# Performance work log

Hardware: AMD Instinct MI355X
Metric: run time of the kernel (lower is better)

The kernel has to match this reference:

```python
import jax, jax.numpy as jnp
import numpy as np

N = 50000      # nodes
E = 800000     # edges (avg degree 16)
DIN = 128
DOUT = 128
L = 8          # num GCN2Conv layers
ALPHA = 0.1
THETA = 0.5


def setup_inputs() -> dict:
    key = jax.random.key(0)
    ks = jax.random.split(key, 5)
    x = jax.random.normal(ks[0], (N, DIN), jnp.float32)
    edge_index = jax.random.randint(ks[1], (2, E), 0, N, dtype=jnp.int64)
    # pre-normalized adjacency weights (normalize=False in GCN2Conv -> adj_t already normalized)
    edge_weight = jax.random.uniform(ks[2], (E,), jnp.float32) / 16.0
    W_lin = jax.random.normal(ks[3], (DIN, DOUT), jnp.float32) / np.sqrt(DIN).astype(np.float32)
    b_lin = jnp.zeros((DOUT,), jnp.float32)
    W_convs = jax.random.normal(ks[4], (L, DOUT, DOUT), jnp.float32) / np.sqrt(DOUT).astype(np.float32)
    return {"x": x, "edge_weight": edge_weight, "W_lin": W_lin, "b_lin": b_lin,
            "W_convs": W_convs, "edge_index": edge_index}


def reference(x, edge_weight, W_lin, b_lin, W_convs, edge_index):
    src, dst = edge_index[0], edge_index[1]
    # betas for GCN2Conv layer l (1-indexed): beta_l = log(theta/l + 1)
    betas = np.log(THETA / np.arange(1, L + 1) + 1.0).astype(np.float32)
    # x = lins(x).relu(); dropout p=0 is a no-op
    x0 = jax.nn.relu(x @ W_lin + b_lin)          # [N, DOUT]
    h = x0
    for l in range(L):
        # sparse propagate: agg = A @ h  (SpMM via gather + segment_sum)
        agg = jax.ops.segment_sum(h[src] * edge_weight[:, None], dst, num_segments=N)
        # initial-residual mixing
        m = (1.0 - ALPHA) * agg + ALPHA * x0
        # identity mapping (shared_weights): out = (1-beta)*m + beta*(m @ W)
        h = jax.nn.relu((1.0 - betas[l]) * m + betas[l] * (m @ W_convs[l]))
    return h
```

## Files before the change

kernel.cpp:

```cpp
#include <hip/hip_runtime.h>
#include <math.h>

#define N_NODES 50000
#define N_EDGES 800000
#define DIM 128
#define PAD 120

typedef __attribute__((ext_vector_type(8))) short short8;
typedef __attribute__((ext_vector_type(4))) float floatx4;

__device__ __forceinline__ unsigned short f32_to_bf16(float f) {
    unsigned int u = __float_as_uint(f);
    u += 0x7fffu + ((u >> 16) & 1u);
    return (unsigned short)(u >> 16);
}
__device__ __forceinline__ float bf16_to_f32(unsigned short h) {
    return __uint_as_float((unsigned int)h << 16);
}

__global__ __launch_bounds__(256) void prep(const float* __restrict__ Wlin,
                                            const float* __restrict__ Wcv,
                                            int* __restrict__ cnt,
                                            unsigned short* __restrict__ WTg) {
    int i = blockIdx.x * 256 + threadIdx.x;
    if (i < N_NODES) cnt[i] = 0;
    int m = i >> 14;
    int n = (i >> 7) & 127;
    int k = i & 127;
    float v;
    if (m == 0) {
        v = Wlin[k * 128 + n];
    } else {
        int l = m - 1;
        float beta = logf(0.5f / (float)(l + 1) + 1.0f);
        v = beta * Wcv[(size_t)l * 16384 + k * 128 + n]
            + ((n == k) ? (1.0f - beta) : 0.0f);
    }
    WTg[i] = f32_to_bf16(v);
}

__global__ __launch_bounds__(256) void scatter_pad(const int* __restrict__ src,
                                                   const int* __restrict__ dst,
                                                   const float* __restrict__ ew,
                                                   int* __restrict__ cnt,
                                                   int2* __restrict__ bucket) {
    int e = blockIdx.x * 256 + threadIdx.x;
    if (e < N_EDGES) {
        int d = dst[e];
        int pos = atomicAdd(&cnt[d], 1);
        if (pos < PAD) {
            int2 p; p.x = src[e]; p.y = __float_as_int(ew[e]);
            bucket[(size_t)d * PAD + pos] = p;
        }
    }
}

__global__ __launch_bounds__(256) void gemm_x0(const float* __restrict__ x,
                                               const unsigned short* __restrict__ WTg,
                                               const float* __restrict__ bias,
                                               unsigned short* __restrict__ x0B) {
    __shared__ unsigned short WT[128][136];
    for (int idx = threadIdx.x; idx < 2048; idx += 256) {
        int n = idx >> 4, c = idx & 15;
        *(short8*)(void*)&WT[n][c * 8] =
            *(const short8*)(const void*)(WTg + n * 128 + c * 8);
    }
    __syncthreads();
    int wave = threadIdx.x >> 6;
    int lane = threadIdx.x & 63;
    int r0 = (blockIdx.x * 4 + wave) * 16;
    if (r0 >= N_NODES) return;
    int mrow = lane & 15;
    int quad = lane >> 4;
    floatx4 acc[8];
#pragma unroll
    for (int t = 0; t < 8; t++) acc[t] = {0.f, 0.f, 0.f, 0.f};
#pragma unroll
    for (int k0 = 0; k0 < 128; k0 += 32) {
        const float* arow = x + (size_t)(r0 + mrow) * DIM;
        floatx4 alo = *(const floatx4*)(const void*)(arow + k0 + quad * 8);
        floatx4 ahi = *(const floatx4*)(const void*)(arow + k0 + quad * 8 + 4);
        short8 a;
#pragma unroll
        for (int j = 0; j < 4; j++) a[j] = (short)f32_to_bf16(alo[j]);
#pragma unroll
        for (int j = 0; j < 4; j++) a[4 + j] = (short)f32_to_bf16(ahi[j]);
#pragma unroll
        for (int t = 0; t < 8; t++) {
            short8 b = *(const short8*)(const void*)(&WT[t * 16 + mrow][k0 + quad * 8]);
            acc[t] = __builtin_amdgcn_mfma_f32_16x16x32_bf16(a, b, acc[t], 0, 0, 0);
        }
    }
#pragma unroll
    for (int t = 0; t < 8; t++) {
        int col = t * 16 + mrow;
        float bv = bias[col];
#pragma unroll
        for (int i = 0; i < 4; i++) {
            int row = r0 + quad * 4 + i;
            float v = fmaxf(acc[t][i] + bv, 0.f);
            x0B[(size_t)row * DIM + col] = f32_to_bf16(v);
        }
    }
}

__global__ __launch_bounds__(512, 4) void layer_fused(
        const unsigned short* __restrict__ hB,
        const unsigned short* __restrict__ x0B,
        const int* __restrict__ cnt,
        const int2* __restrict__ bucket,
        const unsigned short* __restrict__ WTg,
        float* __restrict__ outF,
        unsigned short* __restrict__ outB) {
    __shared__ unsigned short WT[128][136];
    __shared__ unsigned short M[32][136];
    int tid = threadIdx.x;
    for (int idx = tid; idx < 2048; idx += 512) {
        int n = idx >> 4, c = idx & 15;
        *(short8*)(void*)&WT[n][c * 8] =
            *(const short8*)(const void*)(WTg + n * 128 + c * 8);
    }
    int wave = tid >> 6;
    int lane = tid & 63;
    int eg = lane >> 4;
    int fb = (lane & 15) * 8;
    int r0 = blockIdx.x * 32;

    for (int s = 0; s < 4; s++) {
        int row = (wave << 2) + s;
        int node = r0 + row;
        float acc[8] = {0.f, 0.f, 0.f, 0.f, 0.f, 0.f, 0.f, 0.f};
        if (node < N_NODES) {
            int end = min(cnt[node], PAD);
            if (end > 0) {
                const int2* ep = bucket + (size_t)node * PAD;
                int last = end - 1;
                for (int i = 0; i < end; i += 16) {
                    int i0 = i + eg, i1 = i0 + 4, i2 = i0 + 8, i3 = i0 + 12;
                    int2 e0 = ep[min(i0, last)];
                    int2 e1 = ep[min(i1, last)];
                    int2 e2 = ep[min(i2, last)];
                    int2 e3 = ep[min(i3, last)];
                    short8 r0v = *(const short8*)(const void*)(hB + (size_t)e0.x * DIM + fb);
                    short8 r1v = *(const short8*)(const void*)(hB + (size_t)e1.x * DIM + fb);
                    short8 r2v = *(const short8*)(const void*)(hB + (size_t)e2.x * DIM + fb);
                    short8 r3v = *(const short8*)(const void*)(hB + (size_t)e3.x * DIM + fb);
                    float w0 = (i0 < end) ? __int_as_float(e0.y) : 0.f;
                    float w1 = (i1 < end) ? __int_as_float(e1.y) : 0.f;
                    float w2 = (i2 < end) ? __int_as_float(e2.y) : 0.f;
                    float w3 = (i3 < end) ? __int_as_float(e3.y) : 0.f;
#pragma unroll
                    for (int j = 0; j < 8; j++) {
                        acc[j] = fmaf(w0, bf16_to_f32((unsigned short)r0v[j]), acc[j]);
                        acc[j] = fmaf(w1, bf16_to_f32((unsigned short)r1v[j]), acc[j]);
                        acc[j] = fmaf(w2, bf16_to_f32((unsigned short)r2v[j]), acc[j]);
                        acc[j] = fmaf(w3, bf16_to_f32((unsigned short)r3v[j]), acc[j]);
                    }
                }
            }
        }
#pragma unroll
        for (int j = 0; j < 8; j++) {
            acc[j] += __shfl_down(acc[j], 32);
            acc[j] += __shfl_down(acc[j], 16);
        }
        if (lane < 16) {
            short8 o;
            if (node < N_NODES) {
                short8 xv = *(const short8*)(const void*)(x0B + (size_t)node * DIM + fb);
#pragma unroll
                for (int j = 0; j < 8; j++)
                    o[j] = (short)f32_to_bf16(0.9f * acc[j]
                                              + 0.1f * bf16_to_f32((unsigned short)xv[j]));
            } else {
#pragma unroll
                for (int j = 0; j < 8; j++) o[j] = 0;
            }
            *(short8*)(void*)&M[row][fb] = o;
        }
    }
    __syncthreads();

    int mrow = lane & 15;
    int quad = lane >> 4;
    int rt = wave >> 2;
    int ctb = (wave & 3) * 2;
    floatx4 acc2[2];
    acc2[0] = {0.f, 0.f, 0.f, 0.f};
    acc2[1] = {0.f, 0.f, 0.f, 0.f};
#pragma unroll
    for (int k0 = 0; k0 < 128; k0 += 32) {
        short8 a = *(const short8*)(const void*)(&M[rt * 16 + mrow][k0 + quad * 8]);
#pragma unroll
        for (int t = 0; t < 2; t++) {
            short8 b = *(const short8*)(const void*)(&WT[(ctb + t) * 16 + mrow][k0 + quad * 8]);
            acc2[t] = __builtin_amdgcn_mfma_f32_16x16x32_bf16(a, b, acc2[t], 0, 0, 0);
        }
    }
#pragma unroll
    for (int t = 0; t < 2; t++) {
        int col = (ctb + t) * 16 + mrow;
#pragma unroll
        for (int i = 0; i < 4; i++) {
            int row = r0 + rt * 16 + quad * 4 + i;
            if (row < N_NODES) {
                float v = fmaxf(acc2[t][i], 0.f);
                size_t off = (size_t)row * DIM + col;
                if (outF) outF[off] = v;
                if (outB) outB[off] = f32_to_bf16(v);
            }
        }
    }
}


extern "C" void kernel_launch(void* const* d_in, const int* in_sizes, int n_in,
                              void* d_out, int out_size, void* d_ws, size_t ws_size,
                              hipStream_t stream) {
    const float* x    = (const float*)d_in[0];
    const float* ew   = (const float*)d_in[1];
    const float* Wlin = (const float*)d_in[2];
    const float* blin = (const float*)d_in[3];
    const float* Wcv  = (const float*)d_in[4];
    const int* eidx = (const int*)d_in[5];
    const int* esrc = eidx;
    const int* edst = eidx + N_EDGES;
    float* out = (float*)d_out;

    char* ws = (char*)d_ws;
    unsigned short* x0B = (unsigned short*)(ws);
    unsigned short* hA  = (unsigned short*)(ws + 12800000);
    unsigned short* hB2 = (unsigned short*)(ws + 25600000);
    int* cnt            = (int*)(ws + 38400000);
    int2* bucket        = (int2*)(ws + 38600064);
    unsigned short* WTg = (unsigned short*)(ws + 86600064);

    prep<<<576, 256, 0, stream>>>(Wlin, Wcv, cnt, WTg);

    scatter_pad<<<(N_EDGES + 255) / 256, 256, 0, stream>>>(esrc, edst, ew, cnt, bucket);

    gemm_x0<<<(N_NODES + 63) / 64, 256, 0, stream>>>(x, WTg, blin, x0B);

    const unsigned short* hin = x0B;
    for (int l = 0; l < 8; l++) {
        unsigned short* hout = (l == 7) ? nullptr : ((l & 1) ? hB2 : hA);
        layer_fused<<<1563, 512, 0, stream>>>(hin, x0B, cnt, bucket,
                                              WTg + (size_t)(1 + l) * 16384,
                                              (l == 7) ? out : nullptr, hout);
        hin = hout;
    }
}
```

Before: 470.6 us.

## Build padded CSR buckets via two-pass binning by destination node block

Replaces the single per-edge atomic scatter into per-node padded buckets with a two-stage approach. Edges are first binned into groups of 64 destination nodes using global atomics. A second kernel then scatters each bin into the per-node buckets using shared-memory atomics. The intent is to cut global atomic contention and scattered writes during graph preprocessing, at the cost of an extra kernel launch and an intermediate buffer aliased onto hA. It also packs the local destination into the high bits of src, which assumes src < 65536 (true for N=50000), and it silently drops edges if a bin exceeds 1536 entries.

```diff
diff --git a/kernel.cpp b/kernel.cpp
--- a/kernel.cpp
+++ b/kernel.cpp
@@ -6,6 +6,11 @@
 #define DIM 128
 #define PAD 120
 
+#define BIN_SHIFT 6
+#define BIN_NODES 64
+#define N_BINS 782
+#define BIN_CAP 1536
+
 typedef __attribute__((ext_vector_type(8))) short short8;
 typedef __attribute__((ext_vector_type(4))) float floatx4;
 
@@ -20,10 +25,10 @@
 
 __global__ __launch_bounds__(256) void prep(const float* __restrict__ Wlin,
                                             const float* __restrict__ Wcv,
-                                            int* __restrict__ cnt,
+                                            int* __restrict__ bc,
                                             unsigned short* __restrict__ WTg) {
     int i = blockIdx.x * 256 + threadIdx.x;
-    if (i < N_NODES) cnt[i] = 0;
+    if (i < N_BINS) bc[i] = 0;
     int m = i >> 14;
     int n = (i >> 7) & 127;
     int k = i & 127;
@@ -39,20 +44,48 @@
     WTg[i] = f32_to_bf16(v);
 }
 
-__global__ __launch_bounds__(256) void scatter_pad(const int* __restrict__ src,
-                                                   const int* __restrict__ dst,
-                                                   const float* __restrict__ ew,
-                                                   int* __restrict__ cnt,
-                                                   int2* __restrict__ bucket) {
+__global__ __launch_bounds__(256) void bin_edges(const int* __restrict__ src,
+                                                 const int* __restrict__ dst,
+                                                 const float* __restrict__ ew,
+                                                 int* __restrict__ bc,
+                                                 int2* __restrict__ binbuf) {
     int e = blockIdx.x * 256 + threadIdx.x;
     if (e < N_EDGES) {
         int d = dst[e];
-        int pos = atomicAdd(&cnt[d], 1);
+        int bin = d >> BIN_SHIFT;
+        int pos = atomicAdd(&bc[bin], 1);
+        if (pos < BIN_CAP) {
+            int2 p;
+            p.x = src[e] | ((d & (BIN_NODES - 1)) << 16);
+            p.y = __float_as_int(ew[e]);
+            binbuf[(size_t)bin * BIN_CAP + pos] = p;
+        }
+    }
+}
+
+__global__ __launch_bounds__(256) void bin_scatter(const int* __restrict__ bc,
+                                                   const int2* __restrict__ binbuf,
+                                                   int* __restrict__ cnt,
+                                                   int2* __restrict__ bucket) {
+    __shared__ int c[BIN_NODES];
+    int b = blockIdx.x;
+    int tid = threadIdx.x;
+    if (tid < BIN_NODES) c[tid] = 0;
+    __syncthreads();
+    int n = min(bc[b], BIN_CAP);
+    int base = b << BIN_SHIFT;
+    for (int i = tid; i < n; i += 256) {
+        int2 p = binbuf[(size_t)b * BIN_CAP + i];
+        int dloc = (p.x >> 16) & (BIN_NODES - 1);
+        int pos = atomicAdd(&c[dloc], 1);
         if (pos < PAD) {
-            int2 p; p.x = src[e]; p.y = __float_as_int(ew[e]);
-            bucket[(size_t)d * PAD + pos] = p;
-        }
-    }
+            int2 q; q.x = p.x & 0xFFFF; q.y = p.y;
+            bucket[(size_t)(base + dloc) * PAD + pos] = q;
+        }
+    }
+    __syncthreads();
+    if (tid < BIN_NODES && base + tid < N_NODES)
+        cnt[base + tid] = min(c[tid], PAD);
 }
 
 __global__ __launch_bounds__(256) void gemm_x0(const float* __restrict__ x,
@@ -234,10 +267,13 @@
     int* cnt            = (int*)(ws + 38400000);
     int2* bucket        = (int2*)(ws + 38600064);
     unsigned short* WTg = (unsigned short*)(ws + 86600064);
-
-    prep<<<576, 256, 0, stream>>>(Wlin, Wcv, cnt, WTg);
-
-    scatter_pad<<<(N_EDGES + 255) / 256, 256, 0, stream>>>(esrc, edst, ew, cnt, bucket);
+    int* bc             = (int*)(ws + 86894976);
+    int2* binbuf        = (int2*)hA;
+
+    prep<<<576, 256, 0, stream>>>(Wlin, Wcv, bc, WTg);
+
+    bin_edges<<<(N_EDGES + 255) / 256, 256, 0, stream>>>(esrc, edst, ew, bc, binbuf);
+    bin_scatter<<<N_BINS, 256, 0, stream>>>(bc, binbuf, cnt, bucket);
 
     gemm_x0<<<(N_NODES + 63) / 64, 256, 0, stream>>>(x, WTg, blin, x0B);
 
```

Result: slower. 625.9 us (+33.0%).

## Replace global-atomic edge scatter with two-pass binned counting sort

Applied to the files above, without the earlier changes.

Replaces the per-edge global atomicAdd scatter into padded per-node buckets with a two-pass approach. The first pass sorts each block's edges into coarse destination bins in shared memory. The second pass gathers each bin across blocks and uses shared-memory atomics to fill buckets and write counts. This is meant to remove global atomic contention and scattered writes, at the cost of an extra pass through a staging buffer. It relies on src and dst fitting in 16 bits, which holds only because N is under 65536, and it reuses the x0 workspace region as the staging buffer.

```diff
diff --git a/kernel.cpp b/kernel.cpp
--- a/kernel.cpp
+++ b/kernel.cpp
@@ -6,6 +6,12 @@
 #define DIM 128
 #define PAD 120
 
+#define EPB 2048
+#define NBLKA 391
+#define BIN_SHIFT 8
+#define NBIN 196
+#define HISTW 197
+
 typedef __attribute__((ext_vector_type(8))) short short8;
 typedef __attribute__((ext_vector_type(4))) float floatx4;
 
@@ -20,10 +26,8 @@
 
 __global__ __launch_bounds__(256) void prep(const float* __restrict__ Wlin,
                                             const float* __restrict__ Wcv,
-                                            int* __restrict__ cnt,
                                             unsigned short* __restrict__ WTg) {
     int i = blockIdx.x * 256 + threadIdx.x;
-    if (i < N_NODES) cnt[i] = 0;
     int m = i >> 14;
     int n = (i >> 7) & 127;
     int k = i & 127;
@@ -39,20 +43,102 @@
     WTg[i] = f32_to_bf16(v);
 }
 
-__global__ __launch_bounds__(256) void scatter_pad(const int* __restrict__ src,
-                                                   const int* __restrict__ dst,
-                                                   const float* __restrict__ ew,
+__global__ __launch_bounds__(256) void bin_sort(const int* __restrict__ src,
+                                                const int* __restrict__ dst,
+                                                const float* __restrict__ ew,
+                                                int* __restrict__ histg,
+                                                int2* __restrict__ binbuf) {
+    __shared__ int hist[NBIN];
+    __shared__ int base[NBIN + 1];
+    __shared__ int cur[NBIN];
+    __shared__ int2 sorted[EPB];
+    int tid = threadIdx.x;
+    int e0 = blockIdx.x * EPB;
+    if (tid < NBIN) hist[tid] = 0;
+    __syncthreads();
+    for (int i = tid; i < EPB; i += 256) {
+        int e = e0 + i;
+        if (e < N_EDGES) atomicAdd(&hist[dst[e] >> BIN_SHIFT], 1);
+    }
+    __syncthreads();
+    if (tid < NBIN) base[tid + 1] = hist[tid];
+    if (tid == 0) base[0] = 0;
+    __syncthreads();
+    for (int off = 1; off < NBIN + 1; off <<= 1) {
+        int v = 0;
+        if (tid >= off && tid <= NBIN) v = base[tid - off];
+        __syncthreads();
+        if (tid >= off && tid <= NBIN) base[tid] += v;
+        __syncthreads();
+    }
+    if (tid < NBIN) cur[tid] = base[tid];
+    __syncthreads();
+    for (int i = tid; i < EPB; i += 256) {
+        int e = e0 + i;
+        if (e < N_EDGES) {
+            int d = dst[e];
+            int pos = atomicAdd(&cur[d >> BIN_SHIFT], 1);
+            int2 p;
+            p.x = (src[e] & 0xFFFF) | (d << 16);
+            p.y = __float_as_int(ew[e]);
+            sorted[pos] = p;
+        }
+    }
+    __syncthreads();
+    int total = base[NBIN];
+    for (int k = tid; k < total; k += 256)
+        binbuf[(size_t)blockIdx.x * EPB + k] = sorted[k];
+    if (tid <= NBIN) histg[blockIdx.x * HISTW + tid] = base[tid];
+}
+
+__global__ __launch_bounds__(512) void bin_scatter(const int* __restrict__ histg,
+                                                   const int2* __restrict__ binbuf,
                                                    int* __restrict__ cnt,
                                                    int2* __restrict__ bucket) {
-    int e = blockIdx.x * 256 + threadIdx.x;
-    if (e < N_EDGES) {
-        int d = dst[e];
-        int pos = atomicAdd(&cnt[d], 1);
-        if (pos < PAD) {
-            int2 p; p.x = src[e]; p.y = __float_as_int(ew[e]);
-            bucket[(size_t)d * PAD + pos] = p;
-        }
-    }
+    __shared__ int segstart[NBLKA];
+    __shared__ int pref[NBLKA + 1];
+    __shared__ int c[128];
+    int bin = blockIdx.x >> 1;
+    int half = blockIdx.x & 1;
+    int tid = threadIdx.x;
+    if (tid < 128) c[tid] = 0;
+    if (tid < NBLKA) {
+        int bs = histg[tid * HISTW + bin];
+        int be = histg[tid * HISTW + bin + 1];
+        segstart[tid] = tid * EPB + bs;
+        pref[tid + 1] = be - bs;
+    }
+    if (tid == 0) pref[0] = 0;
+    __syncthreads();
+    for (int off = 1; off < NBLKA + 1; off <<= 1) {
+        int v = 0;
+        if (tid >= off && tid <= NBLKA) v = pref[tid - off];
+        __syncthreads();
+        if (tid >= off && tid <= NBLKA) pref[tid] += v;
+        __syncthreads();
+    }
+    int T = pref[NBLKA];
+    for (int idx = tid; idx < T; idx += 512) {
+        int lo = 0, hi = NBLKA - 1;
+        while (lo < hi) {
+            int mid = (lo + hi + 1) >> 1;
+            if (pref[mid] <= idx) lo = mid; else hi = mid - 1;
+        }
+        int2 p = binbuf[(size_t)segstart[lo] + (idx - pref[lo])];
+        int d = ((unsigned)p.x) >> 16;
+        int dloc = d & ((1 << BIN_SHIFT) - 1);
+        if ((dloc >> 7) == half) {
+            int pos = atomicAdd(&c[dloc & 127], 1);
+            if (pos < PAD) {
+                int2 q; q.x = p.x & 0xFFFF; q.y = p.y;
+                bucket[(size_t)d * PAD + pos] = q;
+            }
+        }
+    }
+    __syncthreads();
+    int node0 = (bin << BIN_SHIFT) + (half << 7);
+    if (tid < 128 && node0 + tid < N_NODES)
+        cnt[node0 + tid] = min(c[tid], PAD);
 }
 
 __global__ __launch_bounds__(256) void gemm_x0(const float* __restrict__ x,
@@ -234,10 +320,13 @@
     int* cnt            = (int*)(ws + 38400000);
     int2* bucket        = (int2*)(ws + 38600064);
     unsigned short* WTg = (unsigned short*)(ws + 86600064);
-
-    prep<<<576, 256, 0, stream>>>(Wlin, Wcv, cnt, WTg);
-
-    scatter_pad<<<(N_EDGES + 255) / 256, 256, 0, stream>>>(esrc, edst, ew, cnt, bucket);
+    int* histg          = (int*)(ws + 86894976);
+    int2* binbuf        = (int2*)ws;
+
+    prep<<<576, 256, 0, stream>>>(Wlin, Wcv, WTg);
+
+    bin_sort<<<NBLKA, 256, 0, stream>>>(esrc, edst, ew, histg, binbuf);
+    bin_scatter<<<NBIN * 2, 512, 0, stream>>>(histg, binbuf, cnt, bucket);
 
     gemm_x0<<<(N_NODES + 63) / 64, 256, 0, stream>>>(x, WTg, blin, x0B);
 
```

Result: faster. 454.9 us (-3.3%).
